# Optimization experiments

Measured on AMD Instinct MI355X. Metric: run time of the kernel, lower is better.

Reference implementation:

```python
import jax, jax.numpy as jnp
import numpy as np

B, S, H = 16, 4096, 1152
GRID = 64  # 64x64 patch grid -> S = GRID*GRID
OUT_LEN = 256  # pooled soft tokens (k = sqrt(S/OUT_LEN) = 4)


def setup_inputs() -> dict:
    key = jax.random.key(0)
    x = jax.random.normal(key, (B, S, H), dtype=jnp.float32)
    i = jnp.arange(S)
    # position_ids[..., 0] = x coord, [..., 1] = y coord on the patch grid
    pos = jnp.stack([i % GRID, i // GRID], axis=-1).astype(jnp.int32)  # [S, 2]
    position_ids = jnp.broadcast_to(pos, (B, S, 2))
    return {"x": x, "position_ids": position_ids, "output_length": OUT_LEN}


def reference(x, position_ids, output_length):
    b, s, h = x.shape
    # zero out padding positions (pos == [-1, -1])
    padding = jnp.all(position_ids == -1, axis=-1)  # [B, S]
    x = jnp.where(padding[..., None], jnp.float32(0.0), x)

    k = int((s // output_length) ** 0.5)
    k2 = k * k

    pos = jnp.maximum(position_ids, 0)
    max_x = jnp.max(pos[..., 0], axis=-1, keepdims=True) + 1  # [B, 1]
    # bucket index of each patch: (x//k) + (max_x//k) * (y//k)
    kidx = pos[..., 0] // k + (max_x // k) * pos[..., 1] // 1 * 0 + (pos[..., 0] // k) * 0 + (pos[..., 0] // k)
    kidx = pos[..., 0] // k + (max_x // k) * (pos[..., 1] // k)  # [B, S]

    # scatter-mean: segment_sum over flattened (batch-offset) bucket ids, / k^2
    seg = (kidx + jnp.arange(b)[:, None] * output_length).reshape(-1)
    pooled = jax.ops.segment_sum(
        x.reshape(b * s, h), seg, num_segments=b * output_length
    ).reshape(b, output_length, h) / jnp.float32(k2)

    root_hidden = jnp.float32(h ** 0.5)
    return pooled * root_hidden
```

## Files before the change

kernel.cpp:

```cpp
#include <hip/hip_runtime.h>


#define BB 16
#define SS 4096
#define HH 1152
#define OUTL 256
#define KK 4
#define K2 16
#define H4 (HH / 4)
#define HP (H4 / 2)

__global__ __launch_bounds__(256) void build_fused(const int* __restrict__ pos,
                                                   int* __restrict__ counts,
                                                   int* __restrict__ rows) {
    int b = blockIdx.x;
    int t = threadIdx.x;
    const int2* p2 = reinterpret_cast<const int2*>(pos) + (size_t)b * SS;

    int m = 0;
    for (int s = t; s < SS; s += 256) {
        int px = p2[s].x;
        if (px > m) m = px;
    }
    __shared__ int red[256];
    red[t] = m;
    __syncthreads();
    for (int w = 128; w > 0; w >>= 1) {
        if (t < w) red[t] = max(red[t], red[t + w]);
        __syncthreads();
    }
    __shared__ int smx;
    if (t == 0) smx = red[0] + 1;

    __shared__ int lcnt[OUTL];
    __shared__ int lrows[OUTL * K2];
    lcnt[t] = 0;
    __syncthreads();
    int mxk = smx / KK;
    for (int s = t; s < SS; s += 256) {
        int2 xy = p2[s];
        if (xy.x == -1 && xy.y == -1) continue;
        int px = max(xy.x, 0), py = max(xy.y, 0);
        int kidx = px / KK + mxk * (py / KK);
        if ((unsigned)kidx < OUTL) {
            int slot = atomicAdd(&lcnt[kidx], 1);
            if (slot < K2) lrows[kidx * K2 + slot] = s;
        }
    }
    __syncthreads();

    counts[b * OUTL + t] = lcnt[t];
    int* rb = rows + (size_t)b * OUTL * K2;
    for (int i = t; i < OUTL * K2; i += 256) rb[i] = lrows[i];
}

__global__ __launch_bounds__(256) void gather_kernel(const float* __restrict__ x,
                                                     const int* __restrict__ counts,
                                                     const int* __restrict__ rows,
                                                     float* __restrict__ out) {
    int idx = blockIdx.x * 256 + threadIdx.x;
    int c2 = idx % HP;
    int bo = idx / HP;
    int b = bo / OUTL;
    int col = c2 * 2;

    const float4* x4 = reinterpret_cast<const float4*>(x) + (size_t)b * SS * H4 + col;
    const int* rl = rows + (size_t)bo * K2;
    int cnt = counts[bo];
    if (cnt > K2) cnt = K2;

    float4 a0 = {0.f, 0.f, 0.f, 0.f};
    float4 a1 = {0.f, 0.f, 0.f, 0.f};
    if (cnt == K2) {
#pragma unroll
        for (int j = 0; j < K2; ++j) {
            const float4* p = x4 + (size_t)rl[j] * H4;
            float4 v0 = p[0], v1 = p[1];
            a0.x += v0.x; a0.y += v0.y; a0.z += v0.z; a0.w += v0.w;
            a1.x += v1.x; a1.y += v1.y; a1.z += v1.z; a1.w += v1.w;
        }
    } else {
        for (int j = 0; j < cnt; ++j) {
            const float4* p = x4 + (size_t)rl[j] * H4;
            float4 v0 = p[0], v1 = p[1];
            a0.x += v0.x; a0.y += v0.y; a0.z += v0.z; a0.w += v0.w;
            a1.x += v1.x; a1.y += v1.y; a1.z += v1.z; a1.w += v1.w;
        }
    }
    const float scale = 2.1213203435596424f;
    float4 r0, r1;
    r0.x = a0.x * scale; r0.y = a0.y * scale; r0.z = a0.z * scale; r0.w = a0.w * scale;
    r1.x = a1.x * scale; r1.y = a1.y * scale; r1.z = a1.z * scale; r1.w = a1.w * scale;
    float4* o4 = reinterpret_cast<float4*>(out) + (size_t)bo * H4 + col;
    o4[0] = r0;
    o4[1] = r1;
}

extern "C" void kernel_launch(void* const* d_in, const int* in_sizes, int n_in,
                              void* d_out, int out_size, void* d_ws, size_t ws_size,
                              hipStream_t stream) {
    const float* x = (const float*)d_in[0];
    const int* pos = (const int*)d_in[1];
    float* out = (float*)d_out;

    int* counts = (int*)d_ws;
    int* rows = counts + BB * OUTL;

    build_fused<<<BB, 256, 0, stream>>>(pos, counts, rows);

    int total = BB * OUTL * HP;
    gather_kernel<<<total / 256, 256, 0, stream>>>(x, counts, rows, out);
}
```

Baseline: 64.98 us.

## Gather four strided float4 per thread, sort row indices, cache positions in registers

The gather kernel now has each thread handle four float4 columns spaced C4 apart, so every thread sums 16 rows × 4 float4 and reads the row list with int4 loads. This gives more memory requests in flight per thread and halves the thread count. The build kernel keeps the position data in registers instead of reading it twice, and insertion-sorts each bucket's row indices so the gathers walk memory in increasing address order. The costs are a per-thread serial sort, more register pressure, and a grid with fewer threads, which may lower occupancy.

```diff
diff --git a/kernel.cpp b/kernel.cpp
--- a/kernel.cpp
+++ b/kernel.cpp
@@ -8,7 +8,7 @@
 #define KK 4
 #define K2 16
 #define H4 (HH / 4)
-#define HP (H4 / 2)
+#define C4 (H4 / 4)
 
 __global__ __launch_bounds__(256) void build_fused(const int* __restrict__ pos,
                                                    int* __restrict__ counts,
@@ -17,11 +17,13 @@
     int t = threadIdx.x;
     const int2* p2 = reinterpret_cast<const int2*>(pos) + (size_t)b * SS;
 
+    int2 r[SS / 256];
+#pragma unroll
+    for (int i = 0; i < SS / 256; ++i) r[i] = p2[t + i * 256];
+
     int m = 0;
-    for (int s = t; s < SS; s += 256) {
-        int px = p2[s].x;
-        if (px > m) m = px;
-    }
+#pragma unroll
+    for (int i = 0; i < SS / 256; ++i) m = max(m, r[i].x);
     __shared__ int red[256];
     red[t] = m;
     __syncthreads();
@@ -29,29 +31,38 @@
         if (t < w) red[t] = max(red[t], red[t + w]);
         __syncthreads();
     }
-    __shared__ int smx;
-    if (t == 0) smx = red[0] + 1;
+    __shared__ int smxk;
+    if (t == 0) smxk = (red[0] + 1) / KK;
 
     __shared__ int lcnt[OUTL];
     __shared__ int lrows[OUTL * K2];
     lcnt[t] = 0;
     __syncthreads();
-    int mxk = smx / KK;
-    for (int s = t; s < SS; s += 256) {
-        int2 xy = p2[s];
+    int mxk = smxk;
+#pragma unroll
+    for (int i = 0; i < SS / 256; ++i) {
+        int2 xy = r[i];
         if (xy.x == -1 && xy.y == -1) continue;
         int px = max(xy.x, 0), py = max(xy.y, 0);
         int kidx = px / KK + mxk * (py / KK);
         if ((unsigned)kidx < OUTL) {
             int slot = atomicAdd(&lcnt[kidx], 1);
-            if (slot < K2) lrows[kidx * K2 + slot] = s;
+            if (slot < K2) lrows[kidx * K2 + slot] = t + i * 256;
         }
     }
     __syncthreads();
 
-    counts[b * OUTL + t] = lcnt[t];
-    int* rb = rows + (size_t)b * OUTL * K2;
-    for (int i = t; i < OUTL * K2; i += 256) rb[i] = lrows[i];
+    int cnt = min(lcnt[t], K2);
+    int v[K2];
+    for (int j = 0; j < cnt; ++j) {
+        int key = lrows[t * K2 + j];
+        int p = j;
+        while (p > 0 && v[p - 1] > key) { v[p] = v[p - 1]; --p; }
+        v[p] = key;
+    }
+    counts[b * OUTL + t] = cnt;
+    int* rb = rows + ((size_t)b * OUTL + t) * K2;
+    for (int j = 0; j < cnt; ++j) rb[j] = v[j];
 }
 
 __global__ __launch_bounds__(256) void gather_kernel(const float* __restrict__ x,
@@ -59,41 +70,45 @@
                                                      const int* __restrict__ rows,
                                                      float* __restrict__ out) {
     int idx = blockIdx.x * 256 + threadIdx.x;
-    int c2 = idx % HP;
-    int bo = idx / HP;
-    int b = bo / OUTL;
-    int col = c2 * 2;
+    int c4 = idx % C4;
+    int bo = idx / C4;
+    int b = bo >> 8;
 
-    const float4* x4 = reinterpret_cast<const float4*>(x) + (size_t)b * SS * H4 + col;
+    const float4* xb = reinterpret_cast<const float4*>(x) + (size_t)b * SS * H4 + c4;
     const int* rl = rows + (size_t)bo * K2;
-    int cnt = counts[bo];
-    if (cnt > K2) cnt = K2;
+    int cnt = min(counts[bo], K2);
 
-    float4 a0 = {0.f, 0.f, 0.f, 0.f};
-    float4 a1 = {0.f, 0.f, 0.f, 0.f};
+    float4 a0 = {0,0,0,0}, a1 = {0,0,0,0}, a2 = {0,0,0,0}, a3 = {0,0,0,0};
     if (cnt == K2) {
+        const int4* rl4 = reinterpret_cast<const int4*>(rl);
+        int4 ra = rl4[0], rb_ = rl4[1], rc = rl4[2], rd = rl4[3];
+        int ridx[K2] = {ra.x, ra.y, ra.z, ra.w, rb_.x, rb_.y, rb_.z, rb_.w,
+                        rc.x, rc.y, rc.z, rc.w, rd.x, rd.y, rd.z, rd.w};
 #pragma unroll
         for (int j = 0; j < K2; ++j) {
-            const float4* p = x4 + (size_t)rl[j] * H4;
-            float4 v0 = p[0], v1 = p[1];
+            const float4* p = xb + (size_t)ridx[j] * H4;
+            float4 v0 = p[0], v1 = p[C4], v2 = p[2 * C4], v3 = p[3 * C4];
             a0.x += v0.x; a0.y += v0.y; a0.z += v0.z; a0.w += v0.w;
             a1.x += v1.x; a1.y += v1.y; a1.z += v1.z; a1.w += v1.w;
+            a2.x += v2.x; a2.y += v2.y; a2.z += v2.z; a2.w += v2.w;
+            a3.x += v3.x; a3.y += v3.y; a3.z += v3.z; a3.w += v3.w;
         }
     } else {
         for (int j = 0; j < cnt; ++j) {
-            const float4* p = x4 + (size_t)rl[j] * H4;
-            float4 v0 = p[0], v1 = p[1];
+            const float4* p = xb + (size_t)rl[j] * H4;
+            float4 v0 = p[0], v1 = p[C4], v2 = p[2 * C4], v3 = p[3 * C4];
             a0.x += v0.x; a0.y += v0.y; a0.z += v0.z; a0.w += v0.w;
             a1.x += v1.x; a1.y += v1.y; a1.z += v1.z; a1.w += v1.w;
+            a2.x += v2.x; a2.y += v2.y; a2.z += v2.z; a2.w += v2.w;
+            a3.x += v3.x; a3.y += v3.y; a3.z += v3.z; a3.w += v3.w;
         }
     }
     const float scale = 2.1213203435596424f;
-    float4 r0, r1;
-    r0.x = a0.x * scale; r0.y = a0.y * scale; r0.z = a0.z * scale; r0.w = a0.w * scale;
-    r1.x = a1.x * scale; r1.y = a1.y * scale; r1.z = a1.z * scale; r1.w = a1.w * scale;
-    float4* o4 = reinterpret_cast<float4*>(out) + (size_t)bo * H4 + col;
-    o4[0] = r0;
-    o4[1] = r1;
+    float4* ob = reinterpret_cast<float4*>(out) + (size_t)bo * H4 + c4;
+#define SC(a) { a.x *= scale; a.y *= scale; a.z *= scale; a.w *= scale; }
+    SC(a0) SC(a1) SC(a2) SC(a3)
+#undef SC
+    ob[0] = a0; ob[C4] = a1; ob[2 * C4] = a2; ob[3 * C4] = a3;
 }
 
 extern "C" void kernel_launch(void* const* d_in, const int* in_sizes, int n_in,
@@ -108,6 +123,6 @@
 
     build_fused<<<BB, 256, 0, stream>>>(pos, counts, rows);
 
-    int total = BB * OUTL * HP;
+    int total = BB * OUTL * C4;
     gather_kernel<<<total / 256, 256, 0, stream>>>(x, counts, rows, out);
 }
```

Measured after the change: 78.40 us. 20.6% more time.
